# Kernel optimization log

Measured on AMD Instinct MI355X. Metric: run time of the kernel, lower is better.

The kernel has to match this reference:

```python
import jax, jax.numpy as jnp
import numpy as np

BN_EPS = 1e-5

def _conv2d(x, w, b, stride, padding, groups=1):
    out = jax.lax.conv_general_dilated(
        x, w, (stride, stride), padding,
        feature_group_count=groups,
        dimension_numbers=('NCHW', 'OIHW', 'NCHW'))
    return out + b[None, :, None, None]

def _bn(x, g, be, m, v):
    # eval-mode BatchNorm2d
    scale = g / jnp.sqrt(v + BN_EPS)
    return (x - m[None, :, None, None]) * scale[None, :, None, None] + be[None, :, None, None]

def _gelu(x):
    return jax.nn.gelu(x, approximate=False)  # torch nn.GELU default = exact erf

def _forward(x, conv0_w, conv0_b, bn0_g, bn0_b, bn0_m, bn0_v,
             dw_w, dw_b, bn1_g, bn1_b, bn1_m, bn1_v,
             pw_w, pw_b, bn2_g, bn2_b, bn2_m, bn2_v,
             lstm_w, lstm_b, fc_w, fc_b):
    B = x.shape[0]
    nh = conv0_w.shape[0]
    # stem: 4x4 stride-4 conv + BN + GELU -> [B, nh, 8, L]
    y = _gelu(_bn(_conv2d(x, conv0_w, conv0_b, 4, 'VALID'),
                  bn0_g, bn0_b, bn0_m, bn0_v))
    D = dw_w.shape[0]
    for i in range(D):  # MicroBlocks: residual depthwise 3x3 then pointwise 1x1
        r = _gelu(_bn(_conv2d(y, dw_w[i][:, None], dw_b[i], 1, [(1, 1), (1, 1)], groups=nh),
                      bn1_g[i], bn1_b[i], bn1_m[i], bn1_v[i]))
        y = y + r
        y = _gelu(_bn(_conv2d(y, pw_w[i][:, :, None, None], pw_b[i], 1, 'VALID'),
                      bn2_g[i], bn2_b[i], bn2_m[i], bn2_v[i]))
    # ConvLSTM: channel dim nh is the time axis; state is [B, F=8, L]
    L = y.shape[3]
    F = lstm_w.shape[0] // 4
    seq = jnp.transpose(y, (1, 0, 2, 3))  # [nh, B, 8, L]
    h0 = jnp.zeros((B, F, L), y.dtype)

    def step(carry, xt):
        h, c = carry
        comb = jnp.concatenate([xt, h], axis=1)  # [B, 16, L]
        # kernel-size-1 Conv1d == per-position matmul
        A = jnp.einsum('oc,bcl->bol', lstm_w, comb) + lstm_b[None, :, None]
        ai, af, ao, ag = jnp.split(A, 4, axis=1)
        nc = jax.nn.sigmoid(af) * c + jax.nn.sigmoid(ai) * jnp.tanh(ag)
        nhd = jax.nn.sigmoid(ao) * jnp.tanh(nc)
        return (nhd, nc), nhd

    _, ys = jax.lax.scan(step, (h0, h0), seq)  # ys: [nh, B, 8, L]
    feat = jnp.transpose(ys, (1, 0, 2, 3)).reshape(B, nh * F, L)
    # adaptive_avg_pool1d to output size L (== input length) is identity;
    # dropout in eval mode is identity.
    logits = jnp.einsum('bcl,nc->bln', feat, fc_w) + fc_b  # [B, L, nclass]
    return logits

def setup_inputs():
    B, W, NH, D, NCLS, F = 32, 1024, 256, 4, 6625, 8
    key = jax.random.key(0)
    ks = jax.random.split(key, 24)
    n = lambda i, shape, s=0.05: jax.random.normal(ks[i], shape, jnp.float32) * s
    return {
        'x': jax.random.normal(ks[0], (B, 3, 32, W), jnp.float32),
        'conv0_w': n(1, (NH, 3, 4, 4)), 'conv0_b': n(2, (NH,)),
        'bn0_g': 1.0 + n(3, (NH,)), 'bn0_b': n(4, (NH,)),
        'bn0_m': n(5, (NH,)), 'bn0_v': 0.5 + jax.random.uniform(ks[6], (NH,), jnp.float32),
        'dw_w': n(7, (D, NH, 3, 3)), 'dw_b': n(8, (D, NH)),
        'bn1_g': 1.0 + n(9, (D, NH)), 'bn1_b': n(10, (D, NH)),
        'bn1_m': n(11, (D, NH)), 'bn1_v': 0.5 + jax.random.uniform(ks[12], (D, NH), jnp.float32),
        'pw_w': n(13, (D, NH, NH)), 'pw_b': n(14, (D, NH)),
        'bn2_g': 1.0 + n(15, (D, NH)), 'bn2_b': n(16, (D, NH)),
        'bn2_m': n(17, (D, NH)), 'bn2_v': 0.5 + jax.random.uniform(ks[18], (D, NH), jnp.float32),
        'lstm_w': n(19, (4 * F, 2 * F), 0.1), 'lstm_b': n(20, (4 * F,)),
        'fc_w': n(21, (NCLS, NH * F), 0.02), 'fc_b': n(22, (NCLS,)),
    }

def reference(x, conv0_w, conv0_b, bn0_g, bn0_b, bn0_m, bn0_v,
              dw_w, dw_b, bn1_g, bn1_b, bn1_m, bn1_v,
              pw_w, pw_b, bn2_g, bn2_b, bn2_m, bn2_v,
              lstm_w, lstm_b, fc_w, fc_b):
    return _forward(x, conv0_w, conv0_b, bn0_g, bn0_b, bn0_m, bn0_v,
                    dw_w, dw_b, bn1_g, bn1_b, bn1_m, bn1_v,
                    pw_w, pw_b, bn2_g, bn2_b, bn2_m, bn2_v,
                    lstm_w, lstm_b, fc_w, fc_b)
```

## Files before the change

kernel.cpp:

```cpp
#include <hip/hip_runtime.h>
#include <hip/hip_bf16.h>
#include <stdint.h>

#define BNEPS 1e-5f

typedef __bf16 bf16x8 __attribute__((ext_vector_type(8)));
typedef float f32x4 __attribute__((ext_vector_type(4)));

__device__ __forceinline__ float gelu_f(float x) {
    return 0.5f * x * (1.0f + erff(x * 0.70710678118654752440f));
}
__device__ __forceinline__ float sigmoid_f(float x) {
    return 1.0f / (1.0f + __expf(-x));
}
__device__ __forceinline__ float tanh_f(float x) {
    x = fminf(fmaxf(x, -15.0f), 15.0f);
    const float e = __expf(2.0f * x);
    return (e - 1.0f) / (e + 1.0f);
}
__device__ __forceinline__ void async16(const void* g, void* l) {
    __builtin_amdgcn_global_load_lds(
        (const __attribute__((address_space(1))) void*)g,
        (__attribute__((address_space(3))) void*)l,
        16, 0, 0);
}

__global__ __launch_bounds__(256)
void stem_kernel(const float* __restrict__ x, const float* __restrict__ w,
                 const float* __restrict__ cb,
                 const float* __restrict__ bg, const float* __restrict__ bb,
                 const float* __restrict__ bm, const float* __restrict__ bv,
                 float* __restrict__ y0)
{
    __shared__ float sw[64 * 48];
    const int ho = blockIdx.x, b = blockIdx.y, co0 = blockIdx.z * 64;
    const int wo = threadIdx.x;
    for (int i = threadIdx.x; i < 64 * 48; i += 256) sw[i] = w[co0 * 48 + i];
    float p[48];
    #pragma unroll
    for (int c = 0; c < 3; ++c)
        #pragma unroll
        for (int kh = 0; kh < 4; ++kh) {
            const float4 q = *reinterpret_cast<const float4*>(
                &x[((size_t)(b * 3 + c) * 32 + ho * 4 + kh) * 1024 + wo * 4]);
            p[c * 16 + kh * 4 + 0] = q.x;
            p[c * 16 + kh * 4 + 1] = q.y;
            p[c * 16 + kh * 4 + 2] = q.z;
            p[c * 16 + kh * 4 + 3] = q.w;
        }
    __syncthreads();
    for (int c2 = 0; c2 < 64; ++c2) {
        const int co = co0 + c2;
        const float* wp = &sw[c2 * 48];
        float a0 = 0.f, a1 = 0.f, a2 = 0.f, a3 = 0.f;
        #pragma unroll
        for (int i = 0; i < 12; ++i) {
            const float4 wq = *reinterpret_cast<const float4*>(&wp[i * 4]);
            a0 += wq.x * p[i * 4 + 0];
            a1 += wq.y * p[i * 4 + 1];
            a2 += wq.z * p[i * 4 + 2];
            a3 += wq.w * p[i * 4 + 3];
        }
        const float acc = (a0 + a1) + (a2 + a3) + cb[co];
        const float sc = bg[co] / sqrtf(bv[co] + BNEPS);
        const float val = (acc - bm[co]) * sc + bb[co];
        y0[((size_t)(b * 256 + co) * 8 + ho) * 256 + wo] = gelu_f(val);
    }
}

__global__ __launch_bounds__(256)
void dw_kernel(const float* __restrict__ y0, const float* __restrict__ dww,
               const float* __restrict__ dwb,
               const float* __restrict__ bg, const float* __restrict__ bb,
               const float* __restrict__ bm, const float* __restrict__ bv,
               __hip_bfloat16* __restrict__ y1)
{
    __shared__ float tile[8][258];
    const int c = blockIdx.x, b = blockIdx.y, t = threadIdx.x;
    const float* src = &y0[(size_t)(b * 256 + c) * 2048];
    #pragma unroll
    for (int r = 0; r < 8; ++r) tile[r][1 + t] = src[r * 256 + t];
    if (t < 8) { tile[t][0] = 0.f; tile[t][257] = 0.f; }
    float w9[9];
    #pragma unroll
    for (int i = 0; i < 9; ++i) w9[i] = dww[c * 9 + i];
    const float bias = dwb[c];
    const float sc = bg[c] / sqrtf(bv[c] + BNEPS);
    const float sb = bb[c] - bm[c] * sc;
    __syncthreads();
    __hip_bfloat16* dst = &y1[(size_t)(b * 256 + c) * 2048];
    #pragma unroll
    for (int r = 0; r < 8; ++r) {
        float acc = bias;
        #pragma unroll
        for (int kh = 0; kh < 3; ++kh) {
            const int rr = r + kh - 1;
            if (rr < 0 || rr > 7) continue;
            acc += w9[kh * 3 + 0] * tile[rr][t] + w9[kh * 3 + 1] * tile[rr][t + 1]
                 + w9[kh * 3 + 2] * tile[rr][t + 2];
        }
        const float val = gelu_f(acc * sc + sb);
        dst[r * 256 + t] = __float2bfloat16(tile[r][t + 1] + val);
    }
}

__global__ __launch_bounds__(256)
void tr_kernel(const __hip_bfloat16* __restrict__ y1, __hip_bfloat16* __restrict__ y1t)
{
    __shared__ __hip_bfloat16 tile[64][65];
    const int hw0 = blockIdx.x * 64, c0 = blockIdx.y * 64, b = blockIdx.z;
    const int tx = threadIdx.x & 63, ty = threadIdx.x >> 6;
    const __hip_bfloat16* src = &y1[((size_t)b * 256 + c0) * 2048 + hw0];
    #pragma unroll
    for (int r = ty; r < 64; r += 4) tile[r][tx] = src[(size_t)r * 2048 + tx];
    __syncthreads();
    __hip_bfloat16* dst = &y1t[((size_t)b * 2048 + hw0) * 256 + c0];
    #pragma unroll
    for (int r = ty; r < 64; r += 4) dst[(size_t)r * 256 + tx] = tile[tx][r];
}

__global__ __launch_bounds__(256)
void gemm_pw_kernel(const __hip_bfloat16* __restrict__ A,
                    const __hip_bfloat16* __restrict__ Bt,
                    float* __restrict__ out, int K, int NT,
                    const float* __restrict__ q0, const float* __restrict__ q1,
                    const float* __restrict__ q2, const float* __restrict__ q3,
                    const float* __restrict__ q4)
{
    __shared__ __hip_bfloat16 sA[2][4096];
    __shared__ __hip_bfloat16 sB[2][4096];
    const int tid = threadIdx.x;
    const int wave = tid >> 6, lane = tid & 63;
    const int m0 = blockIdx.y * 128, n0 = blockIdx.x * 128;

    auto stage = [&](int buf, int kt) {
        const int k0 = kt << 5;
        #pragma unroll
        for (int r = 0; r < 2; ++r) {
            const int e = wave * 1024 + r * 512 + lane * 8;
            const int row = e >> 5, ko = e & 31;
            async16(&A[(size_t)(m0 + row) * K + k0 + ko], &sA[buf][wave * 1024 + r * 512]);
            async16(&Bt[(size_t)(n0 + row) * K + k0 + ko], &sB[buf][wave * 1024 + r * 512]);
        }
    };

    f32x4 acc[4][4];
    #pragma unroll
    for (int i = 0; i < 4; ++i)
        #pragma unroll
        for (int j = 0; j < 4; ++j) acc[i][j] = (f32x4){0.f, 0.f, 0.f, 0.f};

    stage(0, 0);
    const int wm = wave >> 1, wn = wave & 1;
    const int lrow = lane & 15, lgrp = lane >> 4;
    int cur = 0;
    for (int kt = 0; kt < NT; ++kt) {
        __syncthreads();
        if (kt + 1 < NT) stage(cur ^ 1, kt + 1);
        bf16x8 av[4], bw[4];
        #pragma unroll
        for (int i = 0; i < 4; ++i) {
            av[i] = *reinterpret_cast<const bf16x8*>(&sA[cur][(wm * 64 + i * 16 + lrow) * 32 + lgrp * 8]);
            bw[i] = *reinterpret_cast<const bf16x8*>(&sB[cur][(wn * 64 + i * 16 + lrow) * 32 + lgrp * 8]);
        }
        #pragma unroll
        for (int mi = 0; mi < 4; ++mi)
            #pragma unroll
            for (int ni = 0; ni < 4; ++ni)
                acc[mi][ni] = __builtin_amdgcn_mfma_f32_16x16x32_bf16(av[mi], bw[ni], acc[mi][ni], 0, 0, 0);
        cur ^= 1;
    }

    #pragma unroll
    for (int mi = 0; mi < 4; ++mi) {
        const int rowb = m0 + wm * 64 + mi * 16 + lgrp * 4;
        #pragma unroll
        for (int ni = 0; ni < 4; ++ni) {
            const int col = n0 + wn * 64 + ni * 16 + lrow;
            #pragma unroll
            for (int r = 0; r < 4; ++r) {
                const float v = acc[mi][ni][r];
                const int co = rowb + r;
                const float sc = q1[co] / sqrtf(q4[co] + BNEPS);
                const float sb = q2[co] - q3[co] * sc;
                const float val = gelu_f((v + q0[co]) * sc + sb);
                const int b_ = col >> 11, hw = col & 2047;
                out[((size_t)b_ * 256 + co) * 2048 + hw] = val;
            }
        }
    }
}

__global__ __launch_bounds__(512, 2)
void gemm_fc_kernel(const __hip_bfloat16* __restrict__ A,
                    const __hip_bfloat16* __restrict__ Bt,
                    const float* __restrict__ fcb,
                    float* __restrict__ out)
{
    constexpr int K = 2048, NT = 64, NTILE = 26;
    __shared__ __hip_bfloat16 smem[49152];
    const int tid = threadIdx.x, wave = tid >> 6, lane = tid & 63;
    const int wm = wave >> 2, wn = wave & 3;
    const int r = lane & 15, g = lane >> 4;
    const int swzk = (g ^ ((r >> 1) & 3)) * 8;

    const int bid = blockIdx.x;
    const int swz = (bid & 7) * 104 + (bid >> 3);
    const int m0 = (swz / NTILE) * 256;
    const int n0 = (swz % NTILE) * 256;

    auto stageA = [&](int buf, int kt) {
        #pragma unroll
        for (int r2 = 0; r2 < 2; ++r2) {
            const int e = wave * 128 + r2 * 64 + lane;
            const int row = e >> 2, slot = e & 3;
            const int kg = slot ^ ((row >> 1) & 3);
            async16(&A[(size_t)(m0 + row) * K + kt * 32 + kg * 8],
                    &smem[buf * 8192 + wave * 1024 + r2 * 512]);
        }
    };
    auto stageB = [&](int buf, int kt) {
        #pragma unroll
        for (int r2 = 0; r2 < 2; ++r2) {
            const int e = wave * 128 + r2 * 64 + lane;
            const int row = e >> 2, slot = e & 3;
            const int kg = slot ^ ((row >> 1) & 3);
            async16(&Bt[(size_t)(n0 + row) * K + kt * 32 + kg * 8],
                    &smem[24576 + buf * 8192 + wave * 1024 + r2 * 512]);
        }
    };

    f32x4 acc[8][4];
    #pragma unroll
    for (int i = 0; i < 8; ++i)
        #pragma unroll
        for (int j = 0; j < 4; ++j) acc[i][j] = (f32x4){0.f, 0.f, 0.f, 0.f};

    stageA(0, 0); stageB(0, 0);
    stageA(1, 1); stageB(1, 1);

    int bc = 0;
    for (int kt = 0; kt < NT; ++kt) {
        if (kt < NT - 1) asm volatile("s_waitcnt vmcnt(4)" ::: "memory");
        else             asm volatile("s_waitcnt vmcnt(0)" ::: "memory");
        asm volatile("s_barrier" ::: "memory");

        const int bn = (bc + 2 >= 3) ? bc - 1 : bc + 2;
        if (kt + 2 < NT) stageA(bn, kt + 2);

        const __hip_bfloat16* pA = &smem[bc * 8192];
        const __hip_bfloat16* pB = &smem[24576 + bc * 8192];
        bf16x8 av[8];
        #pragma unroll
        for (int mi = 0; mi < 8; ++mi)
            av[mi] = *reinterpret_cast<const bf16x8*>(&pA[(wm * 128 + mi * 16 + r) * 32 + swzk]);
        bf16x8 b0 = *reinterpret_cast<const bf16x8*>(&pB[(wn * 64 + 0 * 16 + r) * 32 + swzk]);
        bf16x8 b1 = *reinterpret_cast<const bf16x8*>(&pB[(wn * 64 + 1 * 16 + r) * 32 + swzk]);

        __builtin_amdgcn_s_setprio(1);
        #pragma unroll
        for (int mi = 0; mi < 8; ++mi) {
            acc[mi][0] = __builtin_amdgcn_mfma_f32_16x16x32_bf16(av[mi], b0, acc[mi][0], 0, 0, 0);
            acc[mi][1] = __builtin_amdgcn_mfma_f32_16x16x32_bf16(av[mi], b1, acc[mi][1], 0, 0, 0);
        }
        __builtin_amdgcn_s_setprio(0);

        if (kt + 2 < NT) stageB(bn, kt + 2);
        bf16x8 b2 = *reinterpret_cast<const bf16x8*>(&pB[(wn * 64 + 2 * 16 + r) * 32 + swzk]);
        bf16x8 b3 = *reinterpret_cast<const bf16x8*>(&pB[(wn * 64 + 3 * 16 + r) * 32 + swzk]);

        __builtin_amdgcn_s_setprio(1);
        #pragma unroll
        for (int mi = 0; mi < 8; ++mi) {
            acc[mi][2] = __builtin_amdgcn_mfma_f32_16x16x32_bf16(av[mi], b2, acc[mi][2], 0, 0, 0);
            acc[mi][3] = __builtin_amdgcn_mfma_f32_16x16x32_bf16(av[mi], b3, acc[mi][3], 0, 0, 0);
        }
        __builtin_amdgcn_s_setprio(0);

        bc = (bc == 2) ? 0 : bc + 1;
    }

    #pragma unroll
    for (int mi = 0; mi < 8; ++mi) {
        const int rowb = m0 + wm * 128 + mi * 16 + g * 4;
        #pragma unroll
        for (int ni = 0; ni < 4; ++ni) {
            const int col = n0 + wn * 64 + ni * 16 + r;
            if (col < 6625) {
                const float bb = fcb[col];
                #pragma unroll
                for (int rr = 0; rr < 4; ++rr)
                    out[(size_t)(rowb + rr) * 6625 + col] = acc[mi][ni][rr] + bb;
            }
        }
    }
}

__global__ __launch_bounds__(256)
void lstm_kernel(const float* __restrict__ y, const float* __restrict__ lw,
                 const float* __restrict__ lb, __hip_bfloat16* __restrict__ Am)
{
    const int gid = blockIdx.x * 256 + threadIdx.x;
    const int f = gid & 7, pos = gid >> 3;
    const int l = pos & 255, b = pos >> 8;
    float W[4][16], bias[4];
    #pragma unroll
    for (int g = 0; g < 4; ++g) {
        #pragma unroll
        for (int j = 0; j < 16; ++j) W[g][j] = lw[(g * 8 + f) * 16 + j];
        bias[g] = lb[g * 8 + f];
    }
    float h = 0.f, c = 0.f;
    const float* xb = y + (size_t)b * 524288 + f * 256 + l;
    __hip_bfloat16* ob = Am + (size_t)pos * 2048 + f;
    float xn = xb[0];
    for (int t = 0; t < 256; ++t) {
        const float xt = xn;
        if (t < 255) xn = xb[(size_t)(t + 1) * 2048];
        float A0 = bias[0], A1 = bias[1], A2 = bias[2], A3 = bias[3];
        #pragma unroll
        for (int j = 0; j < 8; ++j) {
            const float xj = __shfl(xt, j, 8);
            const float hj = __shfl(h, j, 8);
            A0 += W[0][j] * xj + W[0][8 + j] * hj;
            A1 += W[1][j] * xj + W[1][8 + j] * hj;
            A2 += W[2][j] * xj + W[2][8 + j] * hj;
            A3 += W[3][j] * xj + W[3][8 + j] * hj;
        }
        c = sigmoid_f(A1) * c + sigmoid_f(A0) * tanh_f(A3);
        h = sigmoid_f(A2) * tanh_f(c);
        ob[t * 8] = __float2bfloat16(h);
    }
}

__global__ void cvt_pww_kernel(const float* __restrict__ w, __hip_bfloat16* __restrict__ o, int n)
{
    const int i = blockIdx.x * 256 + threadIdx.x;
    if (i < n) o[i] = __float2bfloat16(w[i]);
}
__global__ void cvt_fcw_kernel(const float* __restrict__ w, __hip_bfloat16* __restrict__ o)
{
    const size_t i = (size_t)blockIdx.x * 256 + threadIdx.x;
    const size_t nrow = i >> 11, k = i & 2047;
    o[i] = (nrow < 6625) ? __float2bfloat16(w[nrow * 2048 + k]) : __float2bfloat16(0.0f);
}

extern "C" void kernel_launch(void* const* d_in, const int* in_sizes, int n_in,
                              void* d_out, int out_size, void* d_ws, size_t ws_size,
                              hipStream_t stream)
{
    const float* x       = (const float*)d_in[0];
    const float* conv0_w = (const float*)d_in[1];
    const float* conv0_b = (const float*)d_in[2];
    const float* bn0_g   = (const float*)d_in[3];
    const float* bn0_b   = (const float*)d_in[4];
    const float* bn0_m   = (const float*)d_in[5];
    const float* bn0_v   = (const float*)d_in[6];
    const float* dw_w    = (const float*)d_in[7];
    const float* dw_b    = (const float*)d_in[8];
    const float* bn1_g   = (const float*)d_in[9];
    const float* bn1_b   = (const float*)d_in[10];
    const float* bn1_m   = (const float*)d_in[11];
    const float* bn1_v   = (const float*)d_in[12];
    const float* pw_w    = (const float*)d_in[13];
    const float* pw_b    = (const float*)d_in[14];
    const float* bn2_g   = (const float*)d_in[15];
    const float* bn2_b   = (const float*)d_in[16];
    const float* bn2_m   = (const float*)d_in[17];
    const float* bn2_v   = (const float*)d_in[18];
    const float* lstm_w  = (const float*)d_in[19];
    const float* lstm_b  = (const float*)d_in[20];
    const float* fc_w    = (const float*)d_in[21];
    const float* fc_b    = (const float*)d_in[22];

    char* ws = (char*)d_ws;
    float* y0            = (float*)(ws);
    __hip_bfloat16* y1   = (__hip_bfloat16*)(ws + 67108864);
    __hip_bfloat16* y1t  = (__hip_bfloat16*)(ws + 100663296);
    __hip_bfloat16* fcwb = (__hip_bfloat16*)(ws + 134217728);
    __hip_bfloat16* pwwb = (__hip_bfloat16*)(ws + 161480704);
    __hip_bfloat16* Am   = (__hip_bfloat16*)(ws + 67108864);

    stem_kernel<<<dim3(8, 32, 4), 256, 0, stream>>>(
        x, conv0_w, conv0_b, bn0_g, bn0_b, bn0_m, bn0_v, y0);
    cvt_pww_kernel<<<1024, 256, 0, stream>>>(pw_w, pwwb, 262144);
    cvt_fcw_kernel<<<53248, 256, 0, stream>>>(fc_w, fcwb);

    for (int i = 0; i < 4; ++i) {
        dw_kernel<<<dim3(256, 32), 256, 0, stream>>>(
            y0, dw_w + i * 2304, dw_b + i * 256,
            bn1_g + i * 256, bn1_b + i * 256, bn1_m + i * 256, bn1_v + i * 256, y1);
        tr_kernel<<<dim3(32, 4, 32), 256, 0, stream>>>(y1, y1t);
        gemm_pw_kernel<<<dim3(512, 2), 256, 0, stream>>>(
            pwwb + i * 65536, y1t, y0, 256, 8,
            pw_b + i * 256, bn2_g + i * 256, bn2_b + i * 256, bn2_m + i * 256, bn2_v + i * 256);
    }

    lstm_kernel<<<256, 256, 0, stream>>>(y0, lstm_w, lstm_b, Am);

    gemm_fc_kernel<<<832, 512, 0, stream>>>(Am, fcwb, fc_b, (float*)d_out);
}
```

Measured before the change: 710.9 us.

## Restructure FC GEMM main loop into ping-pong phases with explicit barriers

```diff
diff --git a/kernel.cpp b/kernel.cpp
--- a/kernel.cpp
+++ b/kernel.cpp
@@ -191,7 +191,7 @@
     }
 }
 
-__global__ __launch_bounds__(512, 2)
+__global__ __launch_bounds__(512, 1)
 void gemm_fc_kernel(const __hip_bfloat16* __restrict__ A,
                     const __hip_bfloat16* __restrict__ Bt,
                     const float* __restrict__ fcb,
@@ -238,44 +238,55 @@
 
     stageA(0, 0); stageB(0, 0);
     stageA(1, 1); stageB(1, 1);
+    asm volatile("s_waitcnt vmcnt(4)" ::: "memory");
+    __builtin_amdgcn_s_barrier();
 
     int bc = 0;
     for (int kt = 0; kt < NT; ++kt) {
-        if (kt < NT - 1) asm volatile("s_waitcnt vmcnt(4)" ::: "memory");
-        else             asm volatile("s_waitcnt vmcnt(0)" ::: "memory");
-        asm volatile("s_barrier" ::: "memory");
-
         const int bn = (bc + 2 >= 3) ? bc - 1 : bc + 2;
-        if (kt + 2 < NT) stageA(bn, kt + 2);
-
+        const int tp = (kt + 2 < NT) ? kt + 2 : NT - 1;
         const __hip_bfloat16* pA = &smem[bc * 8192];
         const __hip_bfloat16* pB = &smem[24576 + bc * 8192];
-        bf16x8 av[8];
-        #pragma unroll
-        for (int mi = 0; mi < 8; ++mi)
-            av[mi] = *reinterpret_cast<const bf16x8*>(&pA[(wm * 128 + mi * 16 + r) * 32 + swzk]);
-        bf16x8 b0 = *reinterpret_cast<const bf16x8*>(&pB[(wn * 64 + 0 * 16 + r) * 32 + swzk]);
-        bf16x8 b1 = *reinterpret_cast<const bf16x8*>(&pB[(wn * 64 + 1 * 16 + r) * 32 + swzk]);
-
+
+        bf16x8 alo[4], bv[4];
+        #pragma unroll
+        for (int mi = 0; mi < 4; ++mi)
+            alo[mi] = *reinterpret_cast<const bf16x8*>(&pA[(wm * 128 + mi * 16 + r) * 32 + swzk]);
+        #pragma unroll
+        for (int ni = 0; ni < 4; ++ni)
+            bv[ni] = *reinterpret_cast<const bf16x8*>(&pB[(wn * 64 + ni * 16 + r) * 32 + swzk]);
+        stageA(bn, tp);
+        __builtin_amdgcn_s_barrier();
+        asm volatile("s_waitcnt lgkmcnt(0)" ::: "memory");
+        __builtin_amdgcn_sched_barrier(0);
         __builtin_amdgcn_s_setprio(1);
         #pragma unroll
-        for (int mi = 0; mi < 8; ++mi) {
-            acc[mi][0] = __builtin_amdgcn_mfma_f32_16x16x32_bf16(av[mi], b0, acc[mi][0], 0, 0, 0);
-            acc[mi][1] = __builtin_amdgcn_mfma_f32_16x16x32_bf16(av[mi], b1, acc[mi][1], 0, 0, 0);
-        }
+        for (int mi = 0; mi < 4; ++mi)
+            #pragma unroll
+            for (int ni = 0; ni < 4; ++ni)
+                acc[mi][ni] = __builtin_amdgcn_mfma_f32_16x16x32_bf16(alo[mi], bv[ni], acc[mi][ni], 0, 0, 0);
         __builtin_amdgcn_s_setprio(0);
-
-        if (kt + 2 < NT) stageB(bn, kt + 2);
-        bf16x8 b2 = *reinterpret_cast<const bf16x8*>(&pB[(wn * 64 + 2 * 16 + r) * 32 + swzk]);
-        bf16x8 b3 = *reinterpret_cast<const bf16x8*>(&pB[(wn * 64 + 3 * 16 + r) * 32 + swzk]);
-
+        __builtin_amdgcn_sched_barrier(0);
+        __builtin_amdgcn_s_barrier();
+
+        bf16x8 ahi[4];
+        #pragma unroll
+        for (int mi = 0; mi < 4; ++mi)
+            ahi[mi] = *reinterpret_cast<const bf16x8*>(&pA[(wm * 128 + (mi + 4) * 16 + r) * 32 + swzk]);
+        stageB(bn, tp);
+        __builtin_amdgcn_s_barrier();
+        asm volatile("s_waitcnt lgkmcnt(0)" ::: "memory");
+        __builtin_amdgcn_sched_barrier(0);
         __builtin_amdgcn_s_setprio(1);
         #pragma unroll
-        for (int mi = 0; mi < 8; ++mi) {
-            acc[mi][2] = __builtin_amdgcn_mfma_f32_16x16x32_bf16(av[mi], b2, acc[mi][2], 0, 0, 0);
-            acc[mi][3] = __builtin_amdgcn_mfma_f32_16x16x32_bf16(av[mi], b3, acc[mi][3], 0, 0, 0);
-        }
+        for (int mi = 0; mi < 4; ++mi)
+            #pragma unroll
+            for (int ni = 0; ni < 4; ++ni)
+                acc[mi + 4][ni] = __builtin_amdgcn_mfma_f32_16x16x32_bf16(ahi[mi], bv[ni], acc[mi + 4][ni], 0, 0, 0);
         __builtin_amdgcn_s_setprio(0);
+        __builtin_amdgcn_sched_barrier(0);
+        asm volatile("s_waitcnt vmcnt(4)" ::: "memory");
+        __builtin_amdgcn_s_barrier();
 
         bc = (bc == 2) ? 0 : bc + 1;
     }
@@ -290,7 +301,8 @@
                 const float bb = fcb[col];
                 #pragma unroll
                 for (int rr = 0; rr < 4; ++rr)
-                    out[(size_t)(rowb + rr) * 6625 + col] = acc[mi][ni][rr] + bb;
+                    __builtin_nontemporal_store(acc[mi][ni][rr] + bb,
+                        &out[(size_t)(rowb + rr) * 6625 + col]);
             }
         }
     }
```

Result: slower. 831.2 us (+16.9%).

## Fuse depthwise conv with transpose and deepen FC GEMM pipeline to four stages

Applied to the files above, without the earlier changes.

```diff
diff --git a/kernel.cpp b/kernel.cpp
--- a/kernel.cpp
+++ b/kernel.cpp
@@ -69,54 +69,45 @@
 }
 
 __global__ __launch_bounds__(256)
-void dw_kernel(const float* __restrict__ y0, const float* __restrict__ dww,
-               const float* __restrict__ dwb,
-               const float* __restrict__ bg, const float* __restrict__ bb,
-               const float* __restrict__ bm, const float* __restrict__ bv,
-               __hip_bfloat16* __restrict__ y1)
-{
-    __shared__ float tile[8][258];
-    const int c = blockIdx.x, b = blockIdx.y, t = threadIdx.x;
-    const float* src = &y0[(size_t)(b * 256 + c) * 2048];
-    #pragma unroll
-    for (int r = 0; r < 8; ++r) tile[r][1 + t] = src[r * 256 + t];
-    if (t < 8) { tile[t][0] = 0.f; tile[t][257] = 0.f; }
+void dwtr_kernel(const float* __restrict__ y0, const float* __restrict__ dww,
+                 const float* __restrict__ dwb,
+                 const float* __restrict__ bg, const float* __restrict__ bb,
+                 const float* __restrict__ bm, const float* __restrict__ bv,
+                 __hip_bfloat16* __restrict__ y1t)
+{
+    __shared__ float tile[32 * 537];
+    const int w0 = blockIdx.x * 64, C0 = blockIdx.y * 32, b = blockIdx.z;
+    const int tid = threadIdx.x;
+    for (int i = tid; i < 32 * 8 * 66; i += 256) {
+        const int wl = i % 66;
+        const int hh = (i / 66) & 7;
+        const int c  = i / (66 * 8);
+        const int gw = w0 - 1 + wl;
+        float v = 0.f;
+        if (gw >= 0 && gw < 256)
+            v = y0[(size_t)((b * 256 + C0 + c) * 8 + hh) * 256 + gw];
+        tile[c * 537 + hh * 67 + wl] = v;
+    }
+    const int c = tid & 31, p = tid >> 5;
     float w9[9];
     #pragma unroll
-    for (int i = 0; i < 9; ++i) w9[i] = dww[c * 9 + i];
-    const float bias = dwb[c];
-    const float sc = bg[c] / sqrtf(bv[c] + BNEPS);
-    const float sb = bb[c] - bm[c] * sc;
+    for (int i = 0; i < 9; ++i) w9[i] = dww[(C0 + c) * 9 + i];
+    const float bias = dwb[C0 + c];
+    const float sc = bg[C0 + c] / sqrtf(bv[C0 + c] + BNEPS);
+    const float sb = bb[C0 + c] - bm[C0 + c] * sc;
     __syncthreads();
-    __hip_bfloat16* dst = &y1[(size_t)(b * 256 + c) * 2048];
-    #pragma unroll
-    for (int r = 0; r < 8; ++r) {
+    for (int it = 0; it < 64; ++it) {
+        const int pos = it * 8 + p;
+        const int h = pos >> 6, w = pos & 63;
+        const float* tc = &tile[c * 537 + h * 67 + (w + 1)];
         float acc = bias;
-        #pragma unroll
-        for (int kh = 0; kh < 3; ++kh) {
-            const int rr = r + kh - 1;
-            if (rr < 0 || rr > 7) continue;
-            acc += w9[kh * 3 + 0] * tile[rr][t] + w9[kh * 3 + 1] * tile[rr][t + 1]
-                 + w9[kh * 3 + 2] * tile[rr][t + 2];
-        }
+        if (h > 0) acc += w9[0] * tc[-68] + w9[1] * tc[-67] + w9[2] * tc[-66];
+        acc += w9[3] * tc[-1] + w9[4] * tc[0] + w9[5] * tc[1];
+        if (h < 7) acc += w9[6] * tc[66] + w9[7] * tc[67] + w9[8] * tc[68];
         const float val = gelu_f(acc * sc + sb);
-        dst[r * 256 + t] = __float2bfloat16(tile[r][t + 1] + val);
-    }
-}
-
-__global__ __launch_bounds__(256)
-void tr_kernel(const __hip_bfloat16* __restrict__ y1, __hip_bfloat16* __restrict__ y1t)
-{
-    __shared__ __hip_bfloat16 tile[64][65];
-    const int hw0 = blockIdx.x * 64, c0 = blockIdx.y * 64, b = blockIdx.z;
-    const int tx = threadIdx.x & 63, ty = threadIdx.x >> 6;
-    const __hip_bfloat16* src = &y1[((size_t)b * 256 + c0) * 2048 + hw0];
-    #pragma unroll
-    for (int r = ty; r < 64; r += 4) tile[r][tx] = src[(size_t)r * 2048 + tx];
-    __syncthreads();
-    __hip_bfloat16* dst = &y1t[((size_t)b * 2048 + hw0) * 256 + c0];
-    #pragma unroll
-    for (int r = ty; r < 64; r += 4) dst[(size_t)r * 256 + tx] = tile[tx][r];
+        y1t[((size_t)(b * 2048 + h * 256 + w0 + w)) * 256 + C0 + c] =
+            __float2bfloat16(tc[0] + val);
+    }
 }
 
 __global__ __launch_bounds__(256)
@@ -198,7 +189,7 @@
                     float* __restrict__ out)
 {
     constexpr int K = 2048, NT = 64, NTILE = 26;
-    __shared__ __hip_bfloat16 smem[49152];
+    __shared__ __hip_bfloat16 smem[65536];
     const int tid = threadIdx.x, wave = tid >> 6, lane = tid & 63;
     const int wm = wave >> 2, wn = wave & 3;
     const int r = lane & 15, g = lane >> 4;
@@ -226,7 +217,7 @@
             const int row = e >> 2, slot = e & 3;
             const int kg = slot ^ ((row >> 1) & 3);
             async16(&Bt[(size_t)(n0 + row) * K + kt * 32 + kg * 8],
-                    &smem[24576 + buf * 8192 + wave * 1024 + r2 * 512]);
+                    &smem[32768 + buf * 8192 + wave * 1024 + r2 * 512]);
         }
     };
 
@@ -238,18 +229,20 @@
 
     stageA(0, 0); stageB(0, 0);
     stageA(1, 1); stageB(1, 1);
+    stageA(2, 2); stageB(2, 2);
 
     int bc = 0;
     for (int kt = 0; kt < NT; ++kt) {
-        if (kt < NT - 1) asm volatile("s_waitcnt vmcnt(4)" ::: "memory");
-        else             asm volatile("s_waitcnt vmcnt(0)" ::: "memory");
+        if (kt < NT - 2)      asm volatile("s_waitcnt vmcnt(8)" ::: "memory");
+        else if (kt == NT - 2) asm volatile("s_waitcnt vmcnt(4)" ::: "memory");
+        else                  asm volatile("s_waitcnt vmcnt(0)" ::: "memory");
         asm volatile("s_barrier" ::: "memory");
 
-        const int bn = (bc + 2 >= 3) ? bc - 1 : bc + 2;
-        if (kt + 2 < NT) stageA(bn, kt + 2);
+        const int bn = (bc + 3) & 3;
+        if (kt + 3 < NT) stageA(bn, kt + 3);
 
         const __hip_bfloat16* pA = &smem[bc * 8192];
-        const __hip_bfloat16* pB = &smem[24576 + bc * 8192];
+        const __hip_bfloat16* pB = &smem[32768 + bc * 8192];
         bf16x8 av[8];
         #pragma unroll
         for (int mi = 0; mi < 8; ++mi)
@@ -265,7 +258,7 @@
         }
         __builtin_amdgcn_s_setprio(0);
 
-        if (kt + 2 < NT) stageB(bn, kt + 2);
+        if (kt + 3 < NT) stageB(bn, kt + 3);
         bf16x8 b2 = *reinterpret_cast<const bf16x8*>(&pB[(wn * 64 + 2 * 16 + r) * 32 + swzk]);
         bf16x8 b3 = *reinterpret_cast<const bf16x8*>(&pB[(wn * 64 + 3 * 16 + r) * 32 + swzk]);
 
@@ -277,7 +270,7 @@
         }
         __builtin_amdgcn_s_setprio(0);
 
-        bc = (bc == 2) ? 0 : bc + 1;
+        bc = (bc + 1) & 3;
     }
 
     #pragma unroll
@@ -375,7 +368,6 @@
 
     char* ws = (char*)d_ws;
     float* y0            = (float*)(ws);
-    __hip_bfloat16* y1   = (__hip_bfloat16*)(ws + 67108864);
     __hip_bfloat16* y1t  = (__hip_bfloat16*)(ws + 100663296);
     __hip_bfloat16* fcwb = (__hip_bfloat16*)(ws + 134217728);
     __hip_bfloat16* pwwb = (__hip_bfloat16*)(ws + 161480704);
@@ -387,10 +379,9 @@
     cvt_fcw_kernel<<<53248, 256, 0, stream>>>(fc_w, fcwb);
 
     for (int i = 0; i < 4; ++i) {
-        dw_kernel<<<dim3(256, 32), 256, 0, stream>>>(
+        dwtr_kernel<<<dim3(4, 8, 32), 256, 0, stream>>>(
             y0, dw_w + i * 2304, dw_b + i * 256,
-            bn1_g + i * 256, bn1_b + i * 256, bn1_m + i * 256, bn1_v + i * 256, y1);
-        tr_kernel<<<dim3(32, 4, 32), 256, 0, stream>>>(y1, y1t);
+            bn1_g + i * 256, bn1_b + i * 256, bn1_m + i * 256, bn1_v + i * 256, y1t);
         gemm_pw_kernel<<<dim3(512, 2), 256, 0, stream>>>(
             pwwb + i * 65536, y1t, y0, 256, 8,
             pw_b + i * 256, bn2_g + i * 256, bn2_b + i * 256, bn2_m + i * 256, bn2_v + i * 256);
```

Result: slower. 933.8 us (+31.4%).

## Switch FC GEMM to double-buffered LDS and raise occupancy bound

Applied to the files above, without the earlier changes.

```diff
diff --git a/kernel.cpp b/kernel.cpp
--- a/kernel.cpp
+++ b/kernel.cpp
@@ -191,14 +191,14 @@
     }
 }
 
-__global__ __launch_bounds__(512, 2)
+__global__ __launch_bounds__(512, 4)
 void gemm_fc_kernel(const __hip_bfloat16* __restrict__ A,
                     const __hip_bfloat16* __restrict__ Bt,
                     const float* __restrict__ fcb,
                     float* __restrict__ out)
 {
     constexpr int K = 2048, NT = 64, NTILE = 26;
-    __shared__ __hip_bfloat16 smem[49152];
+    __shared__ __hip_bfloat16 smem[32768];
     const int tid = threadIdx.x, wave = tid >> 6, lane = tid & 63;
     const int wm = wave >> 2, wn = wave & 3;
     const int r = lane & 15, g = lane >> 4;
@@ -226,7 +226,7 @@
             const int row = e >> 2, slot = e & 3;
             const int kg = slot ^ ((row >> 1) & 3);
             async16(&Bt[(size_t)(n0 + row) * K + kt * 32 + kg * 8],
-                    &smem[24576 + buf * 8192 + wave * 1024 + r2 * 512]);
+                    &smem[16384 + buf * 8192 + wave * 1024 + r2 * 512]);
         }
     };
 
@@ -239,45 +239,41 @@
     stageA(0, 0); stageB(0, 0);
     stageA(1, 1); stageB(1, 1);
 
-    int bc = 0;
     for (int kt = 0; kt < NT; ++kt) {
         if (kt < NT - 1) asm volatile("s_waitcnt vmcnt(4)" ::: "memory");
         else             asm volatile("s_waitcnt vmcnt(0)" ::: "memory");
-        asm volatile("s_barrier" ::: "memory");
-
-        const int bn = (bc + 2 >= 3) ? bc - 1 : bc + 2;
-        if (kt + 2 < NT) stageA(bn, kt + 2);
-
-        const __hip_bfloat16* pA = &smem[bc * 8192];
-        const __hip_bfloat16* pB = &smem[24576 + bc * 8192];
-        bf16x8 av[8];
+        __builtin_amdgcn_s_barrier();
+
+        const int cur = kt & 1;
+        const __hip_bfloat16* pA = &smem[cur * 8192];
+        const __hip_bfloat16* pB = &smem[16384 + cur * 8192];
+
+        bf16x8 av[8], bv[4];
         #pragma unroll
         for (int mi = 0; mi < 8; ++mi)
             av[mi] = *reinterpret_cast<const bf16x8*>(&pA[(wm * 128 + mi * 16 + r) * 32 + swzk]);
-        bf16x8 b0 = *reinterpret_cast<const bf16x8*>(&pB[(wn * 64 + 0 * 16 + r) * 32 + swzk]);
-        bf16x8 b1 = *reinterpret_cast<const bf16x8*>(&pB[(wn * 64 + 1 * 16 + r) * 32 + swzk]);
+        #pragma unroll
+        for (int ni = 0; ni < 4; ++ni)
+            bv[ni] = *reinterpret_cast<const bf16x8*>(&pB[(wn * 64 + ni * 16 + r) * 32 + swzk]);
+
+        asm volatile("s_waitcnt lgkmcnt(0)" ::: "memory");
+        __builtin_amdgcn_s_barrier();
+        if (kt + 2 < NT) { stageA(cur, kt + 2); stageB(cur, kt + 2); }
 
         __builtin_amdgcn_s_setprio(1);
         #pragma unroll
         for (int mi = 0; mi < 8; ++mi) {
-            acc[mi][0] = __builtin_amdgcn_mfma_f32_16x16x32_bf16(av[mi], b0, acc[mi][0], 0, 0, 0);
-            acc[mi][1] = __builtin_amdgcn_mfma_f32_16x16x32_bf16(av[mi], b1, acc[mi][1], 0, 0, 0);
+            acc[mi][0] = __builtin_amdgcn_mfma_f32_16x16x32_bf16(av[mi], bv[0], acc[mi][0], 0, 0, 0);
+            acc[mi][1] = __builtin_amdgcn_mfma_f32_16x16x32_bf16(av[mi], bv[1], acc[mi][1], 0, 0, 0);
         }
         __builtin_amdgcn_s_setprio(0);
-
-        if (kt + 2 < NT) stageB(bn, kt + 2);
-        bf16x8 b2 = *reinterpret_cast<const bf16x8*>(&pB[(wn * 64 + 2 * 16 + r) * 32 + swzk]);
-        bf16x8 b3 = *reinterpret_cast<const bf16x8*>(&pB[(wn * 64 + 3 * 16 + r) * 32 + swzk]);
-
         __builtin_amdgcn_s_setprio(1);
         #pragma unroll
         for (int mi = 0; mi < 8; ++mi) {
-            acc[mi][2] = __builtin_amdgcn_mfma_f32_16x16x32_bf16(av[mi], b2, acc[mi][2], 0, 0, 0);
-            acc[mi][3] = __builtin_amdgcn_mfma_f32_16x16x32_bf16(av[mi], b3, acc[mi][3], 0, 0, 0);
+            acc[mi][2] = __builtin_amdgcn_mfma_f32_16x16x32_bf16(av[mi], bv[2], acc[mi][2], 0, 0, 0);
+            acc[mi][3] = __builtin_amdgcn_mfma_f32_16x16x32_bf16(av[mi], bv[3], acc[mi][3], 0, 0, 0);
         }
         __builtin_amdgcn_s_setprio(0);
-
-        bc = (bc == 2) ? 0 : bc + 1;
     }
 
     #pragma unroll
```

After: 2.714 ms. 3.82x slower.
